# Kernel optimization log

Measured on AMD Instinct MI355X. Metric: run time of the kernel, lower is better.

The kernel has to match this reference:

```python
import jax, jax.numpy as jnp
import numpy as np

N_QUBITS = 10
N_LAYERS = 4
NUM_CLASSES = 10
BATCH = 2048
DIM = 1 << N_QUBITS  # 1024 state-vector dimension

# basis-state bit tables (wire w <-> bit position w; any consistent ordering
# yields identical PauliZ expectation values)
_d = np.arange(DIM)
_bits = (_d[None, :] >> np.arange(N_QUBITS)[:, None]) & 1          # [n, D]
_SIGN = jnp.asarray(1.0 - 2.0 * _bits, dtype=jnp.float32)         # [n, D], z_w(d) = +/-1
_ZZ = _SIGN[:-1] * _SIGN[1:]                                       # [n-1, D], z_i*z_{i+1}
# CNOT(control=i, target=i+1) basis permutations (self-inverse)
_CNOT_PERM = [np.where((_d >> i) & 1, _d ^ (1 << (i + 1)), _d) for i in range(N_QUBITS - 1)]


def _apply_ry(state, theta, wire):
    # state: [B, D] complex64, theta: scalar angle, RY = [[c,-s],[s,c]], c=cos(theta/2)
    B, D = state.shape
    lo = 1 << wire
    st = state.reshape(B, D // (2 * lo), 2, lo)
    c = jnp.cos(0.5 * theta)
    s = jnp.sin(0.5 * theta)
    s0, s1 = st[:, :, 0, :], st[:, :, 1, :]
    return jnp.stack([c * s0 - s * s1, s * s0 + c * s1], axis=2).reshape(B, D)


def _circuit(inp, weights):
    # inp: [B, n] rotation angles (pre_net output), weights: [L+1, n]
    B = inp.shape[0]
    # Hadamards on |0...0> -> uniform superposition
    state = jnp.full((B, DIM), DIM ** -0.5, dtype=jnp.complex64)
    # ZZFeatureMap is fully diagonal: RZ(2*x_i) gives phase exp(-1j*x_i*z_i);
    # CNOT-RZ(2*(pi-x_i)*(pi-x_{i+1}))-CNOT gives phase exp(-1j*(pi-x_i)*(pi-x_{i+1})*z_i*z_{i+1})
    ang = inp @ _SIGN + ((np.pi - inp[:, :-1]) * (np.pi - inp[:, 1:])) @ _ZZ  # [B, D]
    state = state * jnp.exp(-1j * ang)
    # RealAmplitudes-style ansatz
    for l in range(N_LAYERS):
        for i in range(N_QUBITS):
            state = _apply_ry(state, weights[l, i], i)
        for p in _CNOT_PERM:
            state = state[:, p]
    for i in range(N_QUBITS):
        state = _apply_ry(state, weights[N_LAYERS, i], i)
    probs = jnp.square(state.real) + jnp.square(state.imag)  # [B, D]
    return probs @ _SIGN.T                                    # [B, n] PauliZ expvals


def setup_inputs() -> dict:
    k = jax.random.split(jax.random.key(0), 5)
    x = jax.random.normal(k[0], (BATCH, N_QUBITS), jnp.float32)
    W_pre = jax.random.normal(k[1], (N_QUBITS, N_QUBITS), jnp.float32) / np.sqrt(N_QUBITS).astype(np.float32)
    b_pre = jnp.zeros((N_QUBITS,), jnp.float32)
    # TorchLayer default init: uniform(0, 2*pi)
    weights = jax.random.uniform(k[2], (N_LAYERS + 1, N_QUBITS), jnp.float32, 0.0, 2.0 * np.pi)
    W_post = jax.random.normal(k[3], (NUM_CLASSES, N_QUBITS), jnp.float32) / np.sqrt(N_QUBITS).astype(np.float32)
    b_post = jnp.zeros((NUM_CLASSES,), jnp.float32)
    return {"x": x, "W_pre": W_pre, "b_pre": b_pre, "weights": weights,
            "W_post": W_post, "b_post": b_post}


def reference(x, W_pre, b_pre, weights, W_post, b_post):
    h = x @ W_pre.T + b_pre          # pre_net
    q = _circuit(h, weights)         # qlayer: batched state-vector simulation
    return q @ W_post.T + b_post     # post_net
```

## Files before the change

kernel.cpp:

```cpp
#include <hip/hip_runtime.h>

#define NQ   10
#define NL   4
#define NCL  10
#define PI_F 3.14159265358979f

__device__ __forceinline__ float bcastf(float v, int l) {
    return __int_as_float(__builtin_amdgcn_readlane(__float_as_int(v), l));
}

template<int M>
__device__ __forceinline__ float xlane(float v) {
    if constexpr (M == 1) {
        return __int_as_float(__builtin_amdgcn_update_dpp(
            __float_as_int(v), __float_as_int(v), 0xB1, 0xF, 0xF, false));
    } else if constexpr (M == 2) {
        return __int_as_float(__builtin_amdgcn_update_dpp(
            __float_as_int(v), __float_as_int(v), 0x4E, 0xF, 0xF, false));
    } else if constexpr (M == 4) {
        return __int_as_float(__builtin_amdgcn_ds_swizzle(
            __float_as_int(v), 0x101F));
    } else if constexpr (M == 8) {
        return __int_as_float(__builtin_amdgcn_update_dpp(
            __float_as_int(v), __float_as_int(v), 0x128, 0xF, 0xF, false));
    } else if constexpr (M == 16) {
        auto r = __builtin_amdgcn_permlane16_swap(
            (unsigned)__float_as_int(v), (unsigned)__float_as_int(v), false, false);
        return __int_as_float((int)(r[0] ^ r[1] ^ (unsigned)__float_as_int(v)));
    } else {
        auto r = __builtin_amdgcn_permlane32_swap(
            (unsigned)__float_as_int(v), (unsigned)__float_as_int(v), false, false);
        return __int_as_float((int)(r[0] ^ r[1] ^ (unsigned)__float_as_int(v)));
    }
}

template<int M>
__device__ __forceinline__ void xwire(float c, float s, int lane,
                                      float (&sr)[16], float (&si)[16]) {
    const float se = (lane & M) ? s : -s;
    #pragma unroll
    for (int r = 0; r < 16; ++r) {
        float tr = xlane<M>(sr[r]);
        float ti = xlane<M>(si[r]);
        sr[r] = fmaf(c, sr[r], se * tr);
        si[r] = fmaf(c, si[r], se * ti);
    }
}

__global__ __launch_bounds__(256)
void qnn_kernel(const float* __restrict__ x,
                const float* __restrict__ W_pre,
                const float* __restrict__ b_pre,
                const float* __restrict__ weights,
                const float* __restrict__ W_post,
                const float* __restrict__ b_post,
                float* __restrict__ out, int batch)
{
    const int lane = threadIdx.x & 63;
    const int b = blockIdx.x * 4 + (threadIdx.x >> 6);
    if (b >= batch) return;

    float cw = 0.0f, sw = 0.0f;
    if (lane < (NL + 1) * NQ) {
        float th = 0.5f * weights[lane];
        __sincosf(th, &sw, &cw);
    }

    float hval = 0.0f;
    if (lane < NQ) {
        hval = b_pre[lane];
        #pragma unroll
        for (int k = 0; k < NQ; ++k)
            hval = fmaf(x[b * NQ + k], W_pre[lane * NQ + k], hval);
    }
    float h[NQ];
    #pragma unroll
    for (int i = 0; i < NQ; ++i) h[i] = bcastf(hval, i);
    float z[NQ - 1];
    #pragma unroll
    for (int i = 0; i < NQ - 1; ++i) z[i] = (PI_F - h[i]) * (PI_F - h[i + 1]);

    float A = 0.0f;
    #pragma unroll
    for (int i = 4; i < NQ; ++i)
        A += ((lane >> (i - 4)) & 1) ? -h[i] : h[i];
    #pragma unroll
    for (int i = 4; i < NQ - 1; ++i)
        A += (((lane >> (i - 4)) ^ (lane >> (i - 3))) & 1) ? -z[i] : z[i];

    float sr[16], si[16];
    #pragma unroll
    for (int r = 0; r < 16; ++r) {
        float ang = A;
        #pragma unroll
        for (int i = 0; i < 4; ++i)
            ang += ((r >> i) & 1) ? -h[i] : h[i];
        #pragma unroll
        for (int i = 0; i < 3; ++i)
            ang += (((r >> i) ^ (r >> (i + 1))) & 1) ? -z[i] : z[i];
        ang += (((r >> 3) ^ lane) & 1) ? -z[3] : z[3];
        float sn, cn;
        __sincosf(ang, &sn, &cn);
        sr[r] = 0.03125f * cn;
        si[r] = -0.03125f * sn;
    }

    const int plbase = (lane ^ (lane << 1)) & 0x3F;
    const int paddr0 = plbase << 2;
    const int paddr1 = (plbase ^ 1) << 2;

    #pragma clang loop unroll(disable)
    for (int l = 0; l <= NL; ++l) {
        if (l > 0) {
            float nr[16], ni[16];
            #pragma unroll
            for (int r = 0; r < 16; ++r) {
                const int rp = (r ^ (r << 1)) & 0xF;
                const int pa = (r < 8) ? paddr0 : paddr1;
                nr[r] = __int_as_float(__builtin_amdgcn_ds_bpermute(pa, __float_as_int(sr[rp])));
                ni[r] = __int_as_float(__builtin_amdgcn_ds_bpermute(pa, __float_as_int(si[rp])));
            }
            #pragma unroll
            for (int r = 0; r < 16; ++r) { sr[r] = nr[r]; si[r] = ni[r]; }
        }

        const int base = l * NQ;

        #pragma unroll
        for (int w = 0; w < 4; ++w) {
            const float c = bcastf(cw, base + w);
            const float s = bcastf(sw, base + w);
            #pragma unroll
            for (int r = 0; r < 16; ++r) {
                if (r & (1 << w)) continue;
                const int q = r | (1 << w);
                float a0 = sr[r], a1 = sr[q];
                sr[r] = fmaf(c, a0, -(s * a1));
                sr[q] = fmaf(s, a0, c * a1);
                float b0 = si[r], b1 = si[q];
                si[r] = fmaf(c, b0, -(s * b1));
                si[q] = fmaf(s, b0, c * b1);
            }
        }

        xwire<1 >(bcastf(cw, base + 4), bcastf(sw, base + 4), lane, sr, si);
        xwire<2 >(bcastf(cw, base + 5), bcastf(sw, base + 5), lane, sr, si);
        xwire<4 >(bcastf(cw, base + 6), bcastf(sw, base + 6), lane, sr, si);
        xwire<8 >(bcastf(cw, base + 7), bcastf(sw, base + 7), lane, sr, si);
        xwire<16>(bcastf(cw, base + 8), bcastf(sw, base + 8), lane, sr, si);
        xwire<32>(bcastf(cw, base + 9), bcastf(sw, base + 9), lane, sr, si);
    }

    float P = 0.0f;
    float pk[NCL];
    #pragma unroll
    for (int k = 0; k < 4; ++k) pk[k] = 0.0f;
    #pragma unroll
    for (int r = 0; r < 16; ++r) {
        float pr = fmaf(sr[r], sr[r], si[r] * si[r]);
        P += pr;
        #pragma unroll
        for (int k = 0; k < 4; ++k)
            pk[k] += ((r >> k) & 1) ? -pr : pr;
    }
    #pragma unroll
    for (int k = 4; k < NCL; ++k)
        pk[k] = ((lane >> (k - 4)) & 1) ? -P : P;
    #pragma unroll
    for (int k = 0; k < NCL; ++k) {
        float v = pk[k];
        v += xlane<1>(v);
        v += xlane<2>(v);
        v += xlane<4>(v);
        v += xlane<8>(v);
        v += xlane<16>(v);
        v += xlane<32>(v);
        pk[k] = v;
    }

    if (lane < NCL) {
        float o = b_post[lane];
        #pragma unroll
        for (int k = 0; k < NCL; ++k)
            o = fmaf(pk[k], W_post[lane * NQ + k], o);
        out[b * NCL + lane] = o;
    }
}

extern "C" void kernel_launch(void* const* d_in, const int* in_sizes, int n_in,
                              void* d_out, int out_size, void* d_ws, size_t ws_size,
                              hipStream_t stream) {
    const float* x       = (const float*)d_in[0];
    const float* W_pre   = (const float*)d_in[1];
    const float* b_pre   = (const float*)d_in[2];
    const float* weights = (const float*)d_in[3];
    const float* W_post  = (const float*)d_in[4];
    const float* b_post  = (const float*)d_in[5];
    float* outp = (float*)d_out;
    int batch = in_sizes[0] / NQ;
    int grid = (batch + 3) / 4;
    qnn_kernel<<<grid, 256, 0, stream>>>(x, W_pre, b_pre, weights, W_post, b_post, outp, batch);
}
```

Before: 28.93 us.

## Split each state vector across two wavefronts with LDS exchange and packed float2 math

Each batch element's 1024-amplitude state now spans two wavefronts (8 complex amplitudes per lane instead of 16). The top wire's rotation and the CNOT permutation exchange halves through shared memory under __syncthreads. Complex pairs are stored as float2 so the compiler can emit packed FMA. The aim is to double the number of waves for more parallelism and latency hiding and to cut register pressure. The cost is block-wide barriers and LDS traffic on every layer, plus a cross-wave reduction at the end.

```diff
diff --git a/kernel.cpp b/kernel.cpp
--- a/kernel.cpp
+++ b/kernel.cpp
@@ -5,8 +5,22 @@
 #define NCL  10
 #define PI_F 3.14159265358979f
 
+typedef float f2 __attribute__((ext_vector_type(2)));
+
 __device__ __forceinline__ float bcastf(float v, int l) {
     return __int_as_float(__builtin_amdgcn_readlane(__float_as_int(v), l));
+}
+
+__device__ __forceinline__ float bperm(int byteaddr, float v) {
+    return __int_as_float(__builtin_amdgcn_ds_bpermute(byteaddr, __float_as_int(v)));
+}
+
+__device__ __forceinline__ f2 fma2(f2 a, f2 b, f2 c) {
+#if __has_builtin(__builtin_elementwise_fma)
+    return __builtin_elementwise_fma(a, b, c);
+#else
+    f2 r; r.x = fmaf(a.x, b.x, c.x); r.y = fmaf(a.y, b.y, c.y); return r;
+#endif
 }
 
 template<int M>
@@ -35,15 +49,18 @@
 }
 
 template<int M>
-__device__ __forceinline__ void xwire(float c, float s, int lane,
-                                      float (&sr)[16], float (&si)[16]) {
+__device__ __forceinline__ f2 xlane2(f2 v) {
+    f2 r; r.x = xlane<M>(v.x); r.y = xlane<M>(v.y); return r;
+}
+
+template<int M>
+__device__ __forceinline__ void xwire2(float c, float s, int lane, f2 (&sc)[8]) {
     const float se = (lane & M) ? s : -s;
-    #pragma unroll
-    for (int r = 0; r < 16; ++r) {
-        float tr = xlane<M>(sr[r]);
-        float ti = xlane<M>(si[r]);
-        sr[r] = fmaf(c, sr[r], se * tr);
-        si[r] = fmaf(c, si[r], se * ti);
+    const f2 c2 = {c, c}, se2 = {se, se};
+    #pragma unroll
+    for (int r = 0; r < 8; ++r) {
+        f2 t = xlane2<M>(sc[r]);
+        sc[r] = fma2(se2, t, c2 * sc[r]);
     }
 }
 
@@ -56,9 +73,16 @@
                 const float* __restrict__ b_post,
                 float* __restrict__ out, int batch)
 {
-    const int lane = threadIdx.x & 63;
-    const int b = blockIdx.x * 4 + (threadIdx.x >> 6);
-    if (b >= batch) return;
+    __shared__ f2 xch[2][2][2][64][8];
+    __shared__ float sq[2][2][NCL];
+
+    const int tid  = threadIdx.x;
+    const int lane = tid & 63;
+    const int wv   = tid >> 6;
+    const int eb   = wv >> 1;
+    const int W    = wv & 1;
+    int b = blockIdx.x * 2 + eb;
+    if (b >= batch) b = batch - 1;
 
     float cw = 0.0f, sw = 0.0f;
     if (lane < (NL + 1) * NQ) {
@@ -82,107 +106,146 @@
 
     float A = 0.0f;
     #pragma unroll
-    for (int i = 4; i < NQ; ++i)
-        A += ((lane >> (i - 4)) & 1) ? -h[i] : h[i];
-    #pragma unroll
-    for (int i = 4; i < NQ - 1; ++i)
-        A += (((lane >> (i - 4)) ^ (lane >> (i - 3))) & 1) ? -z[i] : z[i];
-
-    float sr[16], si[16];
-    #pragma unroll
-    for (int r = 0; r < 16; ++r) {
+    for (int i = 0; i < 6; ++i)
+        A += ((lane >> i) & 1) ? -h[3 + i] : h[3 + i];
+    A += W ? -h[9] : h[9];
+    #pragma unroll
+    for (int j = 0; j < 5; ++j)
+        A += (((lane >> j) ^ (lane >> (j + 1))) & 1) ? -z[3 + j] : z[3 + j];
+    A += ((((lane >> 5) & 1) ^ W) & 1) ? -z[8] : z[8];
+
+    f2 sc[8];
+    #pragma unroll
+    for (int r = 0; r < 8; ++r) {
         float ang = A;
         #pragma unroll
-        for (int i = 0; i < 4; ++i)
+        for (int i = 0; i < 3; ++i)
             ang += ((r >> i) & 1) ? -h[i] : h[i];
-        #pragma unroll
-        for (int i = 0; i < 3; ++i)
-            ang += (((r >> i) ^ (r >> (i + 1))) & 1) ? -z[i] : z[i];
-        ang += (((r >> 3) ^ lane) & 1) ? -z[3] : z[3];
+        ang += ((r ^ (r >> 1)) & 1) ? -z[0] : z[0];
+        ang += (((r >> 1) ^ (r >> 2)) & 1) ? -z[1] : z[1];
+        ang += (((r >> 2) ^ lane) & 1) ? -z[2] : z[2];
         float sn, cn;
         __sincosf(ang, &sn, &cn);
-        sr[r] = 0.03125f * cn;
-        si[r] = -0.03125f * sn;
+        sc[r].x = 0.03125f * cn;
+        sc[r].y = -0.03125f * sn;
     }
 
     const int plbase = (lane ^ (lane << 1)) & 0x3F;
-    const int paddr0 = plbase << 2;
-    const int paddr1 = (plbase ^ 1) << 2;
+    int pp = 0;
 
     #pragma clang loop unroll(disable)
     for (int l = 0; l <= NL; ++l) {
         if (l > 0) {
-            float nr[16], ni[16];
-            #pragma unroll
-            for (int r = 0; r < 16; ++r) {
-                const int rp = (r ^ (r << 1)) & 0xF;
-                const int pa = (r < 8) ? paddr0 : paddr1;
-                nr[r] = __int_as_float(__builtin_amdgcn_ds_bpermute(pa, __float_as_int(sr[rp])));
-                ni[r] = __int_as_float(__builtin_amdgcn_ds_bpermute(pa, __float_as_int(si[rp])));
-            }
-            #pragma unroll
-            for (int r = 0; r < 16; ++r) { sr[r] = nr[r]; si[r] = ni[r]; }
+            f2 tp[8];
+            #pragma unroll
+            for (int r = 0; r < 8; ++r) {
+                const int srr = (r ^ (r << 1)) & 7;
+                const int pa  = (plbase ^ ((r >> 2) & 1)) << 2;
+                tp[r].x = bperm(pa, sc[srr].x);
+                tp[r].y = bperm(pa, sc[srr].y);
+            }
+            if (lane >= 32) {
+                #pragma unroll
+                for (int r = 0; r < 8; ++r) xch[pp][eb][W][lane][r] = tp[r];
+            }
+            __syncthreads();
+            if (lane >= 32) {
+                #pragma unroll
+                for (int r = 0; r < 8; ++r) tp[r] = xch[pp][eb][W ^ 1][lane][r];
+            }
+            pp ^= 1;
+            #pragma unroll
+            for (int r = 0; r < 8; ++r) sc[r] = tp[r];
         }
 
         const int base = l * NQ;
 
         #pragma unroll
-        for (int w = 0; w < 4; ++w) {
+        for (int w = 0; w < 3; ++w) {
             const float c = bcastf(cw, base + w);
             const float s = bcastf(sw, base + w);
-            #pragma unroll
-            for (int r = 0; r < 16; ++r) {
+            const f2 c2 = {c, c}, s2 = {s, s};
+            #pragma unroll
+            for (int r = 0; r < 8; ++r) {
                 if (r & (1 << w)) continue;
                 const int q = r | (1 << w);
-                float a0 = sr[r], a1 = sr[q];
-                sr[r] = fmaf(c, a0, -(s * a1));
-                sr[q] = fmaf(s, a0, c * a1);
-                float b0 = si[r], b1 = si[q];
-                si[r] = fmaf(c, b0, -(s * b1));
-                si[q] = fmaf(s, b0, c * b1);
+                f2 a0 = sc[r], a1 = sc[q];
+                f2 t = s2 * a1;
+                sc[r] = fma2(c2, a0, -t);
+                sc[q] = fma2(s2, a0, c2 * a1);
             }
         }
 
-        xwire<1 >(bcastf(cw, base + 4), bcastf(sw, base + 4), lane, sr, si);
-        xwire<2 >(bcastf(cw, base + 5), bcastf(sw, base + 5), lane, sr, si);
-        xwire<4 >(bcastf(cw, base + 6), bcastf(sw, base + 6), lane, sr, si);
-        xwire<8 >(bcastf(cw, base + 7), bcastf(sw, base + 7), lane, sr, si);
-        xwire<16>(bcastf(cw, base + 8), bcastf(sw, base + 8), lane, sr, si);
-        xwire<32>(bcastf(cw, base + 9), bcastf(sw, base + 9), lane, sr, si);
-    }
-
-    float P = 0.0f;
-    float pk[NCL];
-    #pragma unroll
-    for (int k = 0; k < 4; ++k) pk[k] = 0.0f;
-    #pragma unroll
-    for (int r = 0; r < 16; ++r) {
-        float pr = fmaf(sr[r], sr[r], si[r] * si[r]);
-        P += pr;
-        #pragma unroll
-        for (int k = 0; k < 4; ++k)
-            pk[k] += ((r >> k) & 1) ? -pr : pr;
-    }
-    #pragma unroll
-    for (int k = 4; k < NCL; ++k)
-        pk[k] = ((lane >> (k - 4)) & 1) ? -P : P;
-    #pragma unroll
-    for (int k = 0; k < NCL; ++k) {
-        float v = pk[k];
-        v += xlane<1>(v);
-        v += xlane<2>(v);
-        v += xlane<4>(v);
-        v += xlane<8>(v);
-        v += xlane<16>(v);
-        v += xlane<32>(v);
-        pk[k] = v;
-    }
-
-    if (lane < NCL) {
+        xwire2<1 >(bcastf(cw, base + 3), bcastf(sw, base + 3), lane, sc);
+        xwire2<2 >(bcastf(cw, base + 4), bcastf(sw, base + 4), lane, sc);
+        xwire2<4 >(bcastf(cw, base + 5), bcastf(sw, base + 5), lane, sc);
+        xwire2<8 >(bcastf(cw, base + 6), bcastf(sw, base + 6), lane, sc);
+        xwire2<16>(bcastf(cw, base + 7), bcastf(sw, base + 7), lane, sc);
+        xwire2<32>(bcastf(cw, base + 8), bcastf(sw, base + 8), lane, sc);
+
+        {
+            const float c = bcastf(cw, base + 9);
+            const float s = bcastf(sw, base + 9);
+            #pragma unroll
+            for (int r = 0; r < 8; ++r) xch[pp][eb][W][lane][r] = sc[r];
+            __syncthreads();
+            const float se = W ? s : -s;
+            const f2 c2 = {c, c}, se2 = {se, se};
+            #pragma unroll
+            for (int r = 0; r < 8; ++r) {
+                f2 t = xch[pp][eb][W ^ 1][lane][r];
+                sc[r] = fma2(se2, t, c2 * sc[r]);
+            }
+            pp ^= 1;
+        }
+    }
+
+    float P = 0.0f, p0 = 0.0f, p1 = 0.0f, p2 = 0.0f;
+    #pragma unroll
+    for (int r = 0; r < 8; ++r) {
+        f2 qq = sc[r] * sc[r];
+        float pr = qq.x + qq.y;
+        P  += pr;
+        p0 += (r & 1) ? -pr : pr;
+        p1 += (r & 2) ? -pr : pr;
+        p2 += (r & 4) ? -pr : pr;
+    }
+    #pragma unroll
+    for (int st = 0; st < 6; ++st) {
+        const int m = 1 << st;
+        if (m == 1)  { p0 += xlane<1 >(p0); p1 += xlane<1 >(p1); p2 += xlane<1 >(p2); }
+        if (m == 2)  { p0 += xlane<2 >(p0); p1 += xlane<2 >(p1); p2 += xlane<2 >(p2); }
+        if (m == 4)  { p0 += xlane<4 >(p0); p1 += xlane<4 >(p1); p2 += xlane<4 >(p2); }
+        if (m == 8)  { p0 += xlane<8 >(p0); p1 += xlane<8 >(p1); p2 += xlane<8 >(p2); }
+        if (m == 16) { p0 += xlane<16>(p0); p1 += xlane<16>(p1); p2 += xlane<16>(p2); }
+        if (m == 32) { p0 += xlane<32>(p0); p1 += xlane<32>(p1); p2 += xlane<32>(p2); }
+    }
+    {
+        float t;
+        t = xlane<1 >(P); P = t + ((lane & 1 ) ? -P : P);
+        t = xlane<2 >(P); P = t + ((lane & 2 ) ? -P : P);
+        t = xlane<4 >(P); P = t + ((lane & 4 ) ? -P : P);
+        t = xlane<8 >(P); P = t + ((lane & 8 ) ? -P : P);
+        t = xlane<16>(P); P = t + ((lane & 16) ? -P : P);
+        t = xlane<32>(P); P = t + ((lane & 32) ? -P : P);
+    }
+    if (lane == 0)  sq[eb][W][9] = W ? -P : P;
+    if (lane == 1)  sq[eb][W][3] = P;
+    if (lane == 2)  sq[eb][W][4] = P;
+    if (lane == 4)  sq[eb][W][5] = P;
+    if (lane == 8)  sq[eb][W][6] = P;
+    if (lane == 16) sq[eb][W][7] = P;
+    if (lane == 32) sq[eb][W][8] = P;
+    if (lane == 33) sq[eb][W][0] = p0;
+    if (lane == 34) sq[eb][W][1] = p1;
+    if (lane == 35) sq[eb][W][2] = p2;
+    __syncthreads();
+
+    if (W == 0 && lane < NCL) {
         float o = b_post[lane];
         #pragma unroll
         for (int k = 0; k < NCL; ++k)
-            o = fmaf(pk[k], W_post[lane * NQ + k], o);
+            o = fmaf(sq[eb][0][k] + sq[eb][1][k], W_post[lane * NQ + k], o);
         out[b * NCL + lane] = o;
     }
 }
@@ -198,6 +261,6 @@
     const float* b_post  = (const float*)d_in[5];
     float* outp = (float*)d_out;
     int batch = in_sizes[0] / NQ;
-    int grid = (batch + 3) / 4;
+    int grid = (batch + 1) / 2;
     qnn_kernel<<<grid, 256, 0, stream>>>(x, W_pre, b_pre, weights, W_post, b_post, outp, batch);
 }
```

Result: slower. 33.21 us (+14.8%).

## Pack complex amplitudes into float2 vectors and use Walsh-Hadamard butterfly for Z reductions

Applied to the files above, without the earlier changes.

Stores real and imaginary parts as a two-wide float vector so that the RY rotations can be emitted as packed FMA instructions (v_pk_fma_f32), roughly halving the VALU instruction count in the gate loops. The six lane-dependent PauliZ sums are replaced with a single in-place Walsh-Hadamard butterfly over P followed by readlanes, in place of six separate full wave reductions. The pre-net is now computed redundantly on every lane with scalar-uniform loads instead of a per-lane dot product followed by broadcasts. The cross-lane permutes are still per-component, so the gain depends on whether the compiler actually emits packed math.

```diff
diff --git a/kernel.cpp b/kernel.cpp
--- a/kernel.cpp
+++ b/kernel.cpp
@@ -5,8 +5,22 @@
 #define NCL  10
 #define PI_F 3.14159265358979f
 
+typedef float f2 __attribute__((ext_vector_type(2)));
+
 __device__ __forceinline__ float bcastf(float v, int l) {
     return __int_as_float(__builtin_amdgcn_readlane(__float_as_int(v), l));
+}
+
+__device__ __forceinline__ float bperm(int byteaddr, float v) {
+    return __int_as_float(__builtin_amdgcn_ds_bpermute(byteaddr, __float_as_int(v)));
+}
+
+__device__ __forceinline__ f2 fma2(f2 a, f2 b, f2 c) {
+#if __has_builtin(__builtin_elementwise_fma)
+    return __builtin_elementwise_fma(a, b, c);
+#else
+    f2 r; r.x = fmaf(a.x, b.x, c.x); r.y = fmaf(a.y, b.y, c.y); return r;
+#endif
 }
 
 template<int M>
@@ -35,16 +49,25 @@
 }
 
 template<int M>
-__device__ __forceinline__ void xwire(float c, float s, int lane,
-                                      float (&sr)[16], float (&si)[16]) {
+__device__ __forceinline__ f2 xlane2(f2 v) {
+    f2 r; r.x = xlane<M>(v.x); r.y = xlane<M>(v.y); return r;
+}
+
+template<int M>
+__device__ __forceinline__ void xwire2(float c, float s, int lane, f2 (&sc)[16]) {
     const float se = (lane & M) ? s : -s;
+    const f2 c2 = {c, c}, se2 = {se, se};
     #pragma unroll
     for (int r = 0; r < 16; ++r) {
-        float tr = xlane<M>(sr[r]);
-        float ti = xlane<M>(si[r]);
-        sr[r] = fmaf(c, sr[r], se * tr);
-        si[r] = fmaf(c, si[r], se * ti);
-    }
+        f2 t = xlane2<M>(sc[r]);
+        sc[r] = fma2(se2, t, c2 * sc[r]);
+    }
+}
+
+__device__ __forceinline__ f2 bsum2(f2 v) {
+    v += xlane2<1 >(v); v += xlane2<2 >(v); v += xlane2<4 >(v);
+    v += xlane2<8 >(v); v += xlane2<16>(v); v += xlane2<32>(v);
+    return v;
 }
 
 __global__ __launch_bounds__(256)
@@ -59,6 +82,7 @@
     const int lane = threadIdx.x & 63;
     const int b = blockIdx.x * 4 + (threadIdx.x >> 6);
     if (b >= batch) return;
+    const int bu = __builtin_amdgcn_readfirstlane(b);
 
     float cw = 0.0f, sw = 0.0f;
     if (lane < (NL + 1) * NQ) {
@@ -66,16 +90,18 @@
         __sincosf(th, &sw, &cw);
     }
 
-    float hval = 0.0f;
-    if (lane < NQ) {
-        hval = b_pre[lane];
+    float xv[NQ];
+    #pragma unroll
+    for (int k = 0; k < NQ; ++k) xv[k] = x[bu * NQ + k];
+    float h[NQ];
+    #pragma unroll
+    for (int j = 0; j < NQ; ++j) {
+        float acc = b_pre[j];
         #pragma unroll
         for (int k = 0; k < NQ; ++k)
-            hval = fmaf(x[b * NQ + k], W_pre[lane * NQ + k], hval);
-    }
-    float h[NQ];
-    #pragma unroll
-    for (int i = 0; i < NQ; ++i) h[i] = bcastf(hval, i);
+            acc = fmaf(xv[k], W_pre[j * NQ + k], acc);
+        h[j] = acc;
+    }
     float z[NQ - 1];
     #pragma unroll
     for (int i = 0; i < NQ - 1; ++i) z[i] = (PI_F - h[i]) * (PI_F - h[i + 1]);
@@ -88,7 +114,7 @@
     for (int i = 4; i < NQ - 1; ++i)
         A += (((lane >> (i - 4)) ^ (lane >> (i - 3))) & 1) ? -z[i] : z[i];
 
-    float sr[16], si[16];
+    f2 sc[16];
     #pragma unroll
     for (int r = 0; r < 16; ++r) {
         float ang = A;
@@ -101,8 +127,8 @@
         ang += (((r >> 3) ^ lane) & 1) ? -z[3] : z[3];
         float sn, cn;
         __sincosf(ang, &sn, &cn);
-        sr[r] = 0.03125f * cn;
-        si[r] = -0.03125f * sn;
+        sc[r].x = 0.03125f * cn;
+        sc[r].y = -0.03125f * sn;
     }
 
     const int plbase = (lane ^ (lane << 1)) & 0x3F;
@@ -112,16 +138,16 @@
     #pragma clang loop unroll(disable)
     for (int l = 0; l <= NL; ++l) {
         if (l > 0) {
-            float nr[16], ni[16];
+            f2 np[16];
             #pragma unroll
             for (int r = 0; r < 16; ++r) {
                 const int rp = (r ^ (r << 1)) & 0xF;
                 const int pa = (r < 8) ? paddr0 : paddr1;
-                nr[r] = __int_as_float(__builtin_amdgcn_ds_bpermute(pa, __float_as_int(sr[rp])));
-                ni[r] = __int_as_float(__builtin_amdgcn_ds_bpermute(pa, __float_as_int(si[rp])));
+                np[r].x = bperm(pa, sc[rp].x);
+                np[r].y = bperm(pa, sc[rp].y);
             }
             #pragma unroll
-            for (int r = 0; r < 16; ++r) { sr[r] = nr[r]; si[r] = ni[r]; }
+            for (int r = 0; r < 16; ++r) sc[r] = np[r];
         }
 
         const int base = l * NQ;
@@ -130,59 +156,61 @@
         for (int w = 0; w < 4; ++w) {
             const float c = bcastf(cw, base + w);
             const float s = bcastf(sw, base + w);
+            const f2 c2 = {c, c}, s2 = {s, s};
             #pragma unroll
             for (int r = 0; r < 16; ++r) {
                 if (r & (1 << w)) continue;
                 const int q = r | (1 << w);
-                float a0 = sr[r], a1 = sr[q];
-                sr[r] = fmaf(c, a0, -(s * a1));
-                sr[q] = fmaf(s, a0, c * a1);
-                float b0 = si[r], b1 = si[q];
-                si[r] = fmaf(c, b0, -(s * b1));
-                si[q] = fmaf(s, b0, c * b1);
+                f2 a0 = sc[r], a1 = sc[q];
+                sc[r] = fma2(c2, a0, -(s2 * a1));
+                sc[q] = fma2(s2, a0, c2 * a1);
             }
         }
 
-        xwire<1 >(bcastf(cw, base + 4), bcastf(sw, base + 4), lane, sr, si);
-        xwire<2 >(bcastf(cw, base + 5), bcastf(sw, base + 5), lane, sr, si);
-        xwire<4 >(bcastf(cw, base + 6), bcastf(sw, base + 6), lane, sr, si);
-        xwire<8 >(bcastf(cw, base + 7), bcastf(sw, base + 7), lane, sr, si);
-        xwire<16>(bcastf(cw, base + 8), bcastf(sw, base + 8), lane, sr, si);
-        xwire<32>(bcastf(cw, base + 9), bcastf(sw, base + 9), lane, sr, si);
-    }
-
-    float P = 0.0f;
-    float pk[NCL];
-    #pragma unroll
-    for (int k = 0; k < 4; ++k) pk[k] = 0.0f;
+        xwire2<1 >(bcastf(cw, base + 4), bcastf(sw, base + 4), lane, sc);
+        xwire2<2 >(bcastf(cw, base + 5), bcastf(sw, base + 5), lane, sc);
+        xwire2<4 >(bcastf(cw, base + 6), bcastf(sw, base + 6), lane, sc);
+        xwire2<8 >(bcastf(cw, base + 7), bcastf(sw, base + 7), lane, sc);
+        xwire2<16>(bcastf(cw, base + 8), bcastf(sw, base + 8), lane, sc);
+        xwire2<32>(bcastf(cw, base + 9), bcastf(sw, base + 9), lane, sc);
+    }
+
+    float P = 0.0f, p0 = 0.0f, p1 = 0.0f, p2 = 0.0f, p3 = 0.0f;
     #pragma unroll
     for (int r = 0; r < 16; ++r) {
-        float pr = fmaf(sr[r], sr[r], si[r] * si[r]);
-        P += pr;
-        #pragma unroll
-        for (int k = 0; k < 4; ++k)
-            pk[k] += ((r >> k) & 1) ? -pr : pr;
-    }
-    #pragma unroll
-    for (int k = 4; k < NCL; ++k)
-        pk[k] = ((lane >> (k - 4)) & 1) ? -P : P;
-    #pragma unroll
-    for (int k = 0; k < NCL; ++k) {
-        float v = pk[k];
-        v += xlane<1>(v);
-        v += xlane<2>(v);
-        v += xlane<4>(v);
-        v += xlane<8>(v);
-        v += xlane<16>(v);
-        v += xlane<32>(v);
-        pk[k] = v;
-    }
+        f2 qq = sc[r] * sc[r];
+        float pr = qq.x + qq.y;
+        P  += pr;
+        p0 += (r & 1) ? -pr : pr;
+        p1 += (r & 2) ? -pr : pr;
+        p2 += (r & 4) ? -pr : pr;
+        p3 += (r & 8) ? -pr : pr;
+    }
+    f2 qa = bsum2((f2){p0, p1});
+    f2 qb = bsum2((f2){p2, p3});
+    {
+        float t;
+        t = xlane<1 >(P); P = t + ((lane & 1 ) ? -P : P);
+        t = xlane<2 >(P); P = t + ((lane & 2 ) ? -P : P);
+        t = xlane<4 >(P); P = t + ((lane & 4 ) ? -P : P);
+        t = xlane<8 >(P); P = t + ((lane & 8 ) ? -P : P);
+        t = xlane<16>(P); P = t + ((lane & 16) ? -P : P);
+        t = xlane<32>(P); P = t + ((lane & 32) ? -P : P);
+    }
+    float q[NCL];
+    q[0] = qa.x; q[1] = qa.y; q[2] = qb.x; q[3] = qb.y;
+    q[4] = bcastf(P, 1);
+    q[5] = bcastf(P, 2);
+    q[6] = bcastf(P, 4);
+    q[7] = bcastf(P, 8);
+    q[8] = bcastf(P, 16);
+    q[9] = bcastf(P, 32);
 
     if (lane < NCL) {
         float o = b_post[lane];
         #pragma unroll
         for (int k = 0; k < NCL; ++k)
-            o = fmaf(pk[k], W_post[lane * NQ + k], o);
+            o = fmaf(q[k], W_post[lane * NQ + k], o);
         out[b * NCL + lane] = o;
     }
 }
```

After: 27.99 us. 1.03x faster.
